# Kernel tuning notes

Hardware: AMD Instinct MI355X
Metric: run time of the kernel (lower is better)

## Reference

```python
import jax, jax.numpy as jnp
import numpy as np

EPS = 1e-5

def _bn(z, gamma, beta):
    mu = z.mean(axis=0)
    var = z.var(axis=0)  # biased, matches torch BN normalization
    return (z - mu) * jax.lax.rsqrt(var + EPS) * gamma + beta

def _sage_bn_relu(h, src, dst, n_nodes, Wl, bl, Wr, gamma, beta):
    # SAGEConv (mean aggr): out = lin_l(mean_{j in N(i)} h_j) + lin_r(h_i)
    msg = h[src]                                               # [E, d] gather
    agg = jax.ops.segment_sum(msg, dst, num_segments=n_nodes)  # [N, d]
    cnt = jax.ops.segment_sum(jnp.ones((src.shape[0], 1), h.dtype), dst,
                              num_segments=n_nodes)            # [N, 1]
    agg = jnp.where(cnt > 0, agg / jnp.maximum(cnt, 1.0), 0.0)
    out = agg @ Wl.T + bl + h @ Wr.T
    return jax.nn.relu(_bn(out, gamma, beta))

def setup_inputs() -> dict:
    key = jax.random.key(0)
    N, E, d, out_c, L, U = 50000, 800000, 128, 128, 3, 256
    ks = jax.random.split(key, 16)
    s = 1.0 / np.sqrt(d)
    return {
        "x": jax.random.normal(ks[0], (N, d), jnp.float32),
        "edge_index": jax.random.randint(ks[1], (2, E), 0, N, jnp.int64),
        "atom_mask": jax.random.uniform(ks[2], (N, 1), jnp.float32),
        "u_index": jax.random.randint(ks[3], (U,), 0, N, jnp.int64),
        "lin_l_w": jax.random.uniform(ks[4], (L, d, d), jnp.float32, -s, s),
        "lin_l_b": jax.random.uniform(ks[5], (L, d), jnp.float32, -s, s),
        "lin_r_w": jax.random.uniform(ks[6], (L, d, d), jnp.float32, -s, s),
        "bn_gamma": jnp.ones((L, d), jnp.float32),
        "bn_beta": jnp.zeros((L, d), jnp.float32),
        "ro_w1": jax.random.uniform(ks[7], (d, d), jnp.float32, -s, s),
        "ro_b1": jax.random.uniform(ks[8], (d,), jnp.float32, -s, s),
        "ro_bn_gamma": jnp.ones((d,), jnp.float32),
        "ro_bn_beta": jnp.zeros((d,), jnp.float32),
        "ro_w2": jax.random.uniform(ks[9], (out_c, d), jnp.float32, -s, s),
        "ro_b2": jax.random.uniform(ks[10], (out_c,), jnp.float32, -s, s),
    }

def reference(x, edge_index, atom_mask, u_index, lin_l_w, lin_l_b, lin_r_w,
              bn_gamma, bn_beta, ro_w1, ro_b1, ro_bn_gamma, ro_bn_beta,
              ro_w2, ro_b2):
    N = x.shape[0]
    src, dst = edge_index[0], edge_index[1]
    h = x
    for l in range(lin_l_w.shape[0]):
        h = _sage_bn_relu(h, src, dst, N, lin_l_w[l], lin_l_b[l],
                          lin_r_w[l], bn_gamma[l], bn_beta[l])
    state = h[u_index]                                         # [U, d]
    z = jax.nn.relu(_bn(h @ ro_w1.T + ro_b1, ro_bn_gamma, ro_bn_beta))
    atom = (z @ ro_w2.T + ro_b2) * atom_mask                   # [N, out]
    return (h, atom, state)
```

## Files before the change

### kernel.cpp

```cpp
#include <hip/hip_runtime.h>

#define D 128
#define LDA 136

typedef __attribute__((ext_vector_type(8))) short bf16x8;
typedef __attribute__((ext_vector_type(4))) float f32x4;

__device__ __forceinline__ ushort f2b(float f) {
  union { float f; unsigned u; } a; a.f = f;
  unsigned u = a.u;
  return (ushort)((u + 0x7fffu + ((u >> 16) & 1u)) >> 16);
}
__device__ __forceinline__ float b2f_lo(unsigned v) {
  union { unsigned u; float f; } a; a.u = v << 16; return a.f;
}
__device__ __forceinline__ float b2f_hi(unsigned v) {
  union { unsigned u; float f; } a; a.u = v & 0xffff0000u; return a.f;
}

__global__ void k_cast_pad(const float* __restrict__ s, ushort* __restrict__ d, int n4, int np4) {
  int i = blockIdx.x * blockDim.x + threadIdx.x;
  if (i >= np4) return;
  uint2 pk;
  if (i < n4) {
    float4 v = *(const float4*)&s[i * 4];
    pk.x = (unsigned)f2b(v.x) | ((unsigned)f2b(v.y) << 16);
    pk.y = (unsigned)f2b(v.z) | ((unsigned)f2b(v.w) << 16);
  } else {
    pk = make_uint2(0u, 0u);
  }
  *(uint2*)&d[i * 4] = pk;
}

__global__ void k_castw(const float* __restrict__ wl, const float* __restrict__ wr,
                        const float* __restrict__ w1, const float* __restrict__ w2,
                        ushort* __restrict__ dst, int LDD) {
  int i = blockIdx.x * blockDim.x + threadIdx.x;
  int total = 2 * LDD + 2 * D * D;
  if (i >= total) return;
  float v;
  if (i < LDD) v = wl[i];
  else if (i < 2 * LDD) v = wr[i - LDD];
  else if (i < 2 * LDD + D * D) v = w1[i - 2 * LDD];
  else v = w2[i - 2 * LDD - D * D];
  dst[i] = f2b(v);
}

__global__ void k_histrank(const int* __restrict__ dstI, int* __restrict__ cnt,
                           int* __restrict__ rankdst, int E) {
  int e = blockIdx.x * blockDim.x + threadIdx.x;
  if (e < E) {
    int d = dstI[e];
    int r = atomicAdd(&cnt[d], 1);
    rankdst[e] = (r << 16) | d;
  }
}
__global__ void k_scan1(const int* __restrict__ cnt, int* __restrict__ off,
                        int* __restrict__ bsum, int n) {
  __shared__ int sd[256];
  int t = threadIdx.x;
  int i = blockIdx.x * 256 + t;
  int x = (i < n) ? cnt[i] : 0;
  sd[t] = x;
  __syncthreads();
  for (int s = 1; s < 256; s <<= 1) {
    int v = (t >= s) ? sd[t - s] : 0;
    __syncthreads();
    sd[t] += v;
    __syncthreads();
  }
  if (i < n) off[i] = sd[t] - x;
  if (t == 255) bsum[blockIdx.x] = sd[255];
}
__global__ void k_scan2(const int* __restrict__ bsum, int* __restrict__ boff, int nb) {
  __shared__ int sd[256];
  int t = threadIdx.x;
  int x = (t < nb) ? bsum[t] : 0;
  sd[t] = x;
  __syncthreads();
  for (int s = 1; s < 256; s <<= 1) {
    int v = (t >= s) ? sd[t - s] : 0;
    __syncthreads();
    sd[t] += v;
    __syncthreads();
  }
  if (t < nb) boff[t] = sd[t] - x;
}
__global__ void k_scan3(int* __restrict__ off, const int* __restrict__ boff, int n) {
  int i = blockIdx.x * blockDim.x + threadIdx.x;
  if (i < n) off[i] += boff[i >> 8];
}
__global__ void k_fill(const int* __restrict__ srcI, const int* __restrict__ rankdst,
                       const int* __restrict__ off, int* __restrict__ eidx, int E) {
  int e = blockIdx.x * blockDim.x + threadIdx.x;
  if (e < E) {
    int rd = rankdst[e];
    int d = rd & 0xFFFF;
    eidx[off[d] + (rd >> 16)] = srcI[e];
  }
}

#define ACC8(A, V, B)                                             \
  A[B + 0] += b2f_lo(V.x); A[B + 1] += b2f_hi(V.x);               \
  A[B + 2] += b2f_lo(V.y); A[B + 3] += b2f_hi(V.y);               \
  A[B + 4] += b2f_lo(V.z); A[B + 5] += b2f_hi(V.z);               \
  A[B + 6] += b2f_lo(V.w); A[B + 7] += b2f_hi(V.w);

template <bool AGG>
__global__ __launch_bounds__(1024, 8) void k_fused(
    const ushort* __restrict__ hin, const ushort* __restrict__ Wl,
    const ushort* __restrict__ Wr, const float* __restrict__ bias,
    const int* __restrict__ off, const int* __restrict__ eidx,
    ushort* __restrict__ pre, float* __restrict__ sums, int N, int E) {
  __shared__ ushort aggS[128 * LDA];
  __shared__ float ls[2 * D];
  int t = threadIdx.x;
  int r0 = blockIdx.x * 128;

  if (t < 2 * D) ls[t] = 0.f;

  if (AGG) {
    int lrow = t >> 3;
    int row = r0 + lrow;
    int part = (t & 7) << 4;
    float a[16];
#pragma unroll
    for (int i = 0; i < 16; ++i) a[i] = 0.f;
    int start = 0, end = 0;
    if (row < N) { start = off[row]; end = (row == N - 1) ? E : off[row + 1]; }
    const ushort* hbase = hin + part;
#pragma unroll 2
    for (int e = start; e < end; ++e) {
      int sn = eidx[e];
      const uint4* p = (const uint4*)(hbase + (size_t)sn * D);
      uint4 v0 = p[0], v1 = p[1];
      ACC8(a, v0, 0) ACC8(a, v1, 8)
    }
    int deg = end - start;
    float inv = (deg > 0) ? 1.0f / (float)deg : 0.f;
    unsigned o[8];
#pragma unroll
    for (int i = 0; i < 8; ++i)
      o[i] = (unsigned)f2b(a[2 * i] * inv) | ((unsigned)f2b(a[2 * i + 1] * inv) << 16);
    uint4* dst = (uint4*)&aggS[lrow * LDA + part];
    dst[0] = make_uint4(o[0], o[1], o[2], o[3]);
    dst[1] = make_uint4(o[4], o[5], o[6], o[7]);
  }
  __syncthreads();

  int lane = t & 63;
  int wid = t >> 6;
  int wr = wid >> 2, wc = wid & 3;
  int rw = wr * 32, cw = wc * 32;
  int lr = lane & 15, lk = (lane >> 4) * 8;

  f32x4 acc[2][2];
#pragma unroll
  for (int i = 0; i < 2; ++i)
#pragma unroll
    for (int j = 0; j < 2; ++j) acc[i][j] = (f32x4){0.f, 0.f, 0.f, 0.f};

#pragma unroll
  for (int ks = 0; ks < 4; ++ks) {
    int kb = ks * 32 + lk;
    bf16x8 aA[2], aB[2];
#pragma unroll
    for (int rt = 0; rt < 2; ++rt) {
      if (AGG) {
        aA[rt] = *(const bf16x8*)&aggS[(rw + rt * 16 + lr) * LDA + kb];
        aB[rt] = *(const bf16x8*)&hin[(size_t)(r0 + rw + rt * 16 + lr) * D + kb];
      } else {
        aA[rt] = *(const bf16x8*)&hin[(size_t)(r0 + rw + rt * 16 + lr) * D + kb];
      }
    }
#pragma unroll
    for (int jt = 0; jt < 2; ++jt) {
      bf16x8 b1 = *(const bf16x8*)&Wl[(size_t)(cw + jt * 16 + lr) * D + kb];
      acc[0][jt] = __builtin_amdgcn_mfma_f32_16x16x32_bf16(aA[0], b1, acc[0][jt], 0, 0, 0);
      acc[1][jt] = __builtin_amdgcn_mfma_f32_16x16x32_bf16(aA[1], b1, acc[1][jt], 0, 0, 0);
      if (AGG) {
        bf16x8 b2 = *(const bf16x8*)&Wr[(size_t)(cw + jt * 16 + lr) * D + kb];
        acc[0][jt] = __builtin_amdgcn_mfma_f32_16x16x32_bf16(aB[0], b2, acc[0][jt], 0, 0, 0);
        acc[1][jt] = __builtin_amdgcn_mfma_f32_16x16x32_bf16(aB[1], b2, acc[1][jt], 0, 0, 0);
      }
    }
  }

  int crow = (lane >> 4) * 4;
#pragma unroll
  for (int jt = 0; jt < 2; ++jt) {
    int col = cw + jt * 16 + lr;
    float bv = bias[col];
    float s1 = 0.f, s2 = 0.f;
#pragma unroll
    for (int rt = 0; rt < 2; ++rt) {
      int rbase = r0 + rw + rt * 16 + crow;
#pragma unroll
      for (int rg = 0; rg < 4; ++rg) {
        int row = rbase + rg;
        if (row < N) {
          float v = acc[rt][jt][rg] + bv;
          pre[(size_t)row * D + col] = f2b(v);
          s1 += v; s2 += v * v;
        }
      }
    }
    s1 += __shfl_xor(s1, 16, 64); s1 += __shfl_xor(s1, 32, 64);
    s2 += __shfl_xor(s2, 16, 64); s2 += __shfl_xor(s2, 32, 64);
    if (lane < 16) {
      atomicAdd(&ls[cw + jt * 16 + lane], s1);
      atomicAdd(&ls[D + cw + jt * 16 + lane], s2);
    }
  }
  __syncthreads();
  if (t < 2 * D) atomicAdd(&sums[t], ls[t]);
}

template <bool F32OUT>
__global__ void k_bnrelu(const ushort* __restrict__ pre, const float* __restrict__ sums,
                         const float* __restrict__ gamma, const float* __restrict__ beta,
                         float* __restrict__ fout, ushort* __restrict__ bout,
                         int N, int Np, float invN) {
  int i4 = blockIdx.x * blockDim.x + threadIdx.x;
  if (i4 >= Np * (D / 4)) return;
  int row = i4 >> 5;
  int c4 = (i4 & 31) * 4;
  uint2 pk;
  if (row < N) {
    uint2 pv = *(const uint2*)&pre[(size_t)row * D + c4];
    float4 v = make_float4(b2f_lo(pv.x), b2f_hi(pv.x), b2f_lo(pv.y), b2f_hi(pv.y));
    float4 s = *(const float4*)&sums[c4];
    float4 q = *(const float4*)&sums[D + c4];
    float4 g = *(const float4*)&gamma[c4];
    float4 b = *(const float4*)&beta[c4];
    float mu, var, sc, sh;
    mu = s.x * invN; var = fmaxf(q.x * invN - mu * mu, 0.f);
    sc = g.x * rsqrtf(var + 1e-5f); sh = b.x - mu * sc;
    v.x = fmaxf(fmaf(v.x, sc, sh), 0.f);
    mu = s.y * invN; var = fmaxf(q.y * invN - mu * mu, 0.f);
    sc = g.y * rsqrtf(var + 1e-5f); sh = b.y - mu * sc;
    v.y = fmaxf(fmaf(v.y, sc, sh), 0.f);
    mu = s.z * invN; var = fmaxf(q.z * invN - mu * mu, 0.f);
    sc = g.z * rsqrtf(var + 1e-5f); sh = b.z - mu * sc;
    v.z = fmaxf(fmaf(v.z, sc, sh), 0.f);
    mu = s.w * invN; var = fmaxf(q.w * invN - mu * mu, 0.f);
    sc = g.w * rsqrtf(var + 1e-5f); sh = b.w - mu * sc;
    v.w = fmaxf(fmaf(v.w, sc, sh), 0.f);
    if (F32OUT) *(float4*)&fout[(size_t)row * D + c4] = v;
    pk.x = (unsigned)f2b(v.x) | ((unsigned)f2b(v.y) << 16);
    pk.y = (unsigned)f2b(v.z) | ((unsigned)f2b(v.w) << 16);
  } else {
    pk = make_uint2(0u, 0u);
  }
  *(uint2*)&bout[(size_t)row * D + c4] = pk;
}

__global__ __launch_bounds__(256) void k_mmfin(
    const ushort* __restrict__ A, const ushort* __restrict__ W,
    const float* __restrict__ bias, const float* __restrict__ mask,
    float* __restrict__ out, int N) {
  int t = threadIdx.x;
  int lane = t & 63;
  int wid = t >> 6;
  int wr = wid >> 1, wc = wid & 1;
  int r0 = blockIdx.x * 128 + wr * 64;
  int c0 = wc * 64;
  int lr = lane & 15, lk = (lane >> 4) * 8;

  f32x4 acc[4][4];
#pragma unroll
  for (int i = 0; i < 4; ++i)
#pragma unroll
    for (int j = 0; j < 4; ++j) acc[i][j] = (f32x4){0.f, 0.f, 0.f, 0.f};

#pragma unroll
  for (int ks = 0; ks < 4; ++ks) {
    int kb = ks * 32 + lk;
    bf16x8 a1[4];
#pragma unroll
    for (int rt = 0; rt < 4; ++rt)
      a1[rt] = *(const bf16x8*)&A[(size_t)(r0 + rt * 16 + lr) * D + kb];
#pragma unroll
    for (int jt = 0; jt < 4; ++jt) {
      bf16x8 b1 = *(const bf16x8*)&W[(size_t)(c0 + jt * 16 + lr) * D + kb];
#pragma unroll
      for (int rt = 0; rt < 4; ++rt)
        acc[rt][jt] = __builtin_amdgcn_mfma_f32_16x16x32_bf16(a1[rt], b1, acc[rt][jt], 0, 0, 0);
    }
  }

  int crow = (lane >> 4) * 4;
#pragma unroll
  for (int rt = 0; rt < 4; ++rt) {
    int rbase = r0 + rt * 16 + crow;
#pragma unroll
    for (int jt = 0; jt < 4; ++jt) {
      int col = c0 + jt * 16 + lr;
      float bv = bias[col];
#pragma unroll
      for (int rg = 0; rg < 4; ++rg) {
        int row = rbase + rg;
        if (row < N) {
          float m = mask[row];
          out[(size_t)row * D + col] = (acc[rt][jt][rg] + bv) * m;
        }
      }
    }
  }
}

__global__ void k_gather(const float* __restrict__ h, const int* __restrict__ uidx,
                         float* __restrict__ outp, int U) {
  int u = blockIdx.x;
  int t = threadIdx.x;
  int s = uidx[u];
  *(float4*)&outp[(size_t)u * D + t * 4] = *(const float4*)&h[(size_t)s * D + t * 4];
}

extern "C" void kernel_launch(void* const* d_in, const int* in_sizes, int n_in,
                              void* d_out, int out_size, void* d_ws, size_t ws_size,
                              hipStream_t stream) {
  const float* x        = (const float*)d_in[0];
  const int*   edge     = (const int*)d_in[1];
  const float* amask    = (const float*)d_in[2];
  const int*   uindex   = (const int*)d_in[3];
  const float* lin_l_w  = (const float*)d_in[4];
  const float* lin_l_b  = (const float*)d_in[5];
  const float* lin_r_w  = (const float*)d_in[6];
  const float* bn_gamma = (const float*)d_in[7];
  const float* bn_beta  = (const float*)d_in[8];
  const float* ro_w1    = (const float*)d_in[9];
  const float* ro_b1    = (const float*)d_in[10];
  const float* ro_bng   = (const float*)d_in[11];
  const float* ro_bnb   = (const float*)d_in[12];
  const float* ro_w2    = (const float*)d_in[13];
  const float* ro_b2    = (const float*)d_in[14];

  const int N = in_sizes[0] / D;
  const int E = in_sizes[1] / 2;
  const int U = in_sizes[3];
  const int L = in_sizes[4] / (D * D);
  const int Np = ((N + 127) / 128) * 128;
  const int LDD = L * D * D;

  const int* srcI = edge;
  const int* dstI = edge + E;

  float* outH     = (float*)d_out;
  float* outAtom  = outH + (size_t)N * D;
  float* outState = outAtom + (size_t)N * D;

  char* w = (char*)d_ws;
  ushort* hb   = (ushort*)w; w += (size_t)Np * D * 2;
  ushort* pre  = (ushort*)w; w += (size_t)Np * D * 2;
  ushort* wall = (ushort*)w; w += (size_t)(2 * LDD + 2 * D * D) * 2;
  int*    cnt  = (int*)w;    w += (size_t)N * 4;
  float*  sums = (float*)w;  w += 4 * 2 * D * 4;
  int* off     = (int*)w;    w += (size_t)N * 4;
  int* rankdst = (int*)w;    w += (size_t)E * 4;
  int* eidx    = (int*)w;    w += (size_t)E * 4;
  int* bsum    = (int*)w;    w += 1024;
  int* boff    = (int*)w;    w += 1024;

  ushort* wlb = wall;
  ushort* wrb = wlb + (size_t)LDD;
  ushort* w1b = wrb + (size_t)LDD;
  ushort* w2b = w1b + (size_t)D * D;

  k_cast_pad<<<(Np * D / 4 + 255) / 256, 256, 0, stream>>>(x, hb, N * D / 4, Np * D / 4);
  k_castw<<<(2 * LDD + 2 * D * D + 255) / 256, 256, 0, stream>>>(lin_l_w, lin_r_w, ro_w1, ro_w2, wall, LDD);
  hipMemsetAsync(cnt, 0, (size_t)N * 4 + 4 * 2 * D * 4, stream);

  int nbE = (E + 255) / 256;
  int nbN = (N + 255) / 256;
  k_histrank<<<nbE, 256, 0, stream>>>(dstI, cnt, rankdst, E);
  k_scan1<<<nbN, 256, 0, stream>>>(cnt, off, bsum, N);
  k_scan2<<<1, 256, 0, stream>>>(bsum, boff, nbN);
  k_scan3<<<nbN, 256, 0, stream>>>(off, boff, N);
  k_fill<<<nbE, 256, 0, stream>>>(srcI, rankdst, off, eidx, E);

  const int fusedBlocks = Np / 128;
  const int bnBlocks = (Np * (D / 4) + 255) / 256;
  const float invN = 1.0f / (float)N;

  for (int l = 0; l < L; ++l) {
    float* lsums = sums + (size_t)l * 2 * D;
    k_fused<true><<<fusedBlocks, 1024, 0, stream>>>(
        hb, wlb + (size_t)l * D * D, wrb + (size_t)l * D * D,
        lin_l_b + (size_t)l * D, off, eidx, pre, lsums, N, E);
    if (l == L - 1)
      k_bnrelu<true><<<bnBlocks, 256, 0, stream>>>(pre, lsums, bn_gamma + (size_t)l * D,
                                                   bn_beta + (size_t)l * D, outH, hb, N, Np, invN);
    else
      k_bnrelu<false><<<bnBlocks, 256, 0, stream>>>(pre, lsums, bn_gamma + (size_t)l * D,
                                                    bn_beta + (size_t)l * D, nullptr, hb, N, Np, invN);
  }

  float* rsums = sums + (size_t)L * 2 * D;
  k_fused<false><<<fusedBlocks, 1024, 0, stream>>>(
      hb, w1b, nullptr, ro_b1, off, eidx, pre, rsums, N, E);
  k_bnrelu<false><<<bnBlocks, 256, 0, stream>>>(pre, rsums, ro_bng, ro_bnb, nullptr, hb, N, Np, invN);
  k_mmfin<<<Np / 128, 256, 0, stream>>>(hb, w2b, ro_b2, amask, outAtom, N);
  k_gather<<<U, 32, 0, stream>>>(outH, uindex, outState, U);
}
```

Measured before the change: 324.4 us.

## Merge prep kernels, shrink edge index to u16, halve fused block size

Merges the input cast, weight cast and memset into a single prep kernel, which saves launch overhead. The CSR edge index is stored as 16-bit values, halving the bytes read in the gather loop. The fused SAGE kernel now uses 512 threads per block: each thread aggregates one row slice in four phases, and each wave computes a 32x64 output tile, giving more MFMA work per wave. Storing source indices as ushort silently truncates any node id of 65536 or more. N is 50000 here, so it is correct for these inputs but not in general.

```diff
diff --git a/kernel.cpp b/kernel.cpp
--- a/kernel.cpp
+++ b/kernel.cpp
@@ -18,32 +18,37 @@
   union { unsigned u; float f; } a; a.u = v & 0xffff0000u; return a.f;
 }
 
-__global__ void k_cast_pad(const float* __restrict__ s, ushort* __restrict__ d, int n4, int np4) {
+__global__ void k_prep(const float* __restrict__ x, const float* __restrict__ wl,
+                       const float* __restrict__ wr, const float* __restrict__ w1,
+                       const float* __restrict__ w2, ushort* __restrict__ hb,
+                       ushort* __restrict__ wall, uint4* __restrict__ zr,
+                       int nX4, int npX4, int LDD, int nZero4) {
   int i = blockIdx.x * blockDim.x + threadIdx.x;
-  if (i >= np4) return;
-  uint2 pk;
-  if (i < n4) {
-    float4 v = *(const float4*)&s[i * 4];
-    pk.x = (unsigned)f2b(v.x) | ((unsigned)f2b(v.y) << 16);
-    pk.y = (unsigned)f2b(v.z) | ((unsigned)f2b(v.w) << 16);
-  } else {
-    pk = make_uint2(0u, 0u);
-  }
-  *(uint2*)&d[i * 4] = pk;
-}
-
-__global__ void k_castw(const float* __restrict__ wl, const float* __restrict__ wr,
-                        const float* __restrict__ w1, const float* __restrict__ w2,
-                        ushort* __restrict__ dst, int LDD) {
-  int i = blockIdx.x * blockDim.x + threadIdx.x;
-  int total = 2 * LDD + 2 * D * D;
-  if (i >= total) return;
-  float v;
-  if (i < LDD) v = wl[i];
-  else if (i < 2 * LDD) v = wr[i - LDD];
-  else if (i < 2 * LDD + D * D) v = w1[i - 2 * LDD];
-  else v = w2[i - 2 * LDD - D * D];
-  dst[i] = f2b(v);
+  if (i < npX4) {
+    uint2 pk;
+    if (i < nX4) {
+      float4 v = *(const float4*)&x[i * 4];
+      pk.x = (unsigned)f2b(v.x) | ((unsigned)f2b(v.y) << 16);
+      pk.y = (unsigned)f2b(v.z) | ((unsigned)f2b(v.w) << 16);
+    } else {
+      pk = make_uint2(0u, 0u);
+    }
+    *(uint2*)&hb[i * 4] = pk;
+    return;
+  }
+  int j = i - npX4;
+  int W = 2 * LDD + 2 * D * D;
+  if (j < W) {
+    float v;
+    if (j < LDD) v = wl[j];
+    else if (j < 2 * LDD) v = wr[j - LDD];
+    else if (j < 2 * LDD + D * D) v = w1[j - 2 * LDD];
+    else v = w2[j - 2 * LDD - D * D];
+    wall[j] = f2b(v);
+    return;
+  }
+  int z = j - W;
+  if (z < nZero4) zr[z] = make_uint4(0u, 0u, 0u, 0u);
 }
 
 __global__ void k_histrank(const int* __restrict__ dstI, int* __restrict__ cnt,
@@ -91,12 +96,12 @@
   if (i < n) off[i] += boff[i >> 8];
 }
 __global__ void k_fill(const int* __restrict__ srcI, const int* __restrict__ rankdst,
-                       const int* __restrict__ off, int* __restrict__ eidx, int E) {
+                       const int* __restrict__ off, ushort* __restrict__ eidx, int E) {
   int e = blockIdx.x * blockDim.x + threadIdx.x;
   if (e < E) {
     int rd = rankdst[e];
     int d = rd & 0xFFFF;
-    eidx[off[d] + (rd >> 16)] = srcI[e];
+    eidx[off[d] + (rd >> 16)] = (ushort)srcI[e];
   }
 }
 
@@ -107,10 +112,10 @@
   A[B + 6] += b2f_lo(V.w); A[B + 7] += b2f_hi(V.w);
 
 template <bool AGG>
-__global__ __launch_bounds__(1024, 8) void k_fused(
+__global__ __launch_bounds__(512) void k_fused(
     const ushort* __restrict__ hin, const ushort* __restrict__ Wl,
     const ushort* __restrict__ Wr, const float* __restrict__ bias,
-    const int* __restrict__ off, const int* __restrict__ eidx,
+    const int* __restrict__ off, const ushort* __restrict__ eidx,
     ushort* __restrict__ pre, float* __restrict__ sums, int N, int E) {
   __shared__ ushort aggS[128 * LDA];
   __shared__ float ls[2 * D];
@@ -120,45 +125,46 @@
   if (t < 2 * D) ls[t] = 0.f;
 
   if (AGG) {
-    int lrow = t >> 3;
+    int lrow = t >> 2;
     int row = r0 + lrow;
-    int part = (t & 7) << 4;
-    float a[16];
-#pragma unroll
-    for (int i = 0; i < 16; ++i) a[i] = 0.f;
+    int sub = (t & 3) << 3;
     int start = 0, end = 0;
     if (row < N) { start = off[row]; end = (row == N - 1) ? E : off[row + 1]; }
-    const ushort* hbase = hin + part;
-#pragma unroll 2
-    for (int e = start; e < end; ++e) {
-      int sn = eidx[e];
-      const uint4* p = (const uint4*)(hbase + (size_t)sn * D);
-      uint4 v0 = p[0], v1 = p[1];
-      ACC8(a, v0, 0) ACC8(a, v1, 8)
-    }
     int deg = end - start;
     float inv = (deg > 0) ? 1.0f / (float)deg : 0.f;
-    unsigned o[8];
-#pragma unroll
-    for (int i = 0; i < 8; ++i)
-      o[i] = (unsigned)f2b(a[2 * i] * inv) | ((unsigned)f2b(a[2 * i + 1] * inv) << 16);
-    uint4* dst = (uint4*)&aggS[lrow * LDA + part];
-    dst[0] = make_uint4(o[0], o[1], o[2], o[3]);
-    dst[1] = make_uint4(o[4], o[5], o[6], o[7]);
+#pragma unroll
+    for (int ph = 0; ph < 4; ++ph) {
+      const ushort* hbase = hin + ph * 32 + sub;
+      float a[8];
+#pragma unroll
+      for (int i = 0; i < 8; ++i) a[i] = 0.f;
+#pragma unroll 2
+      for (int e = start; e < end; ++e) {
+        int sn = eidx[e];
+        uint4 v = *(const uint4*)(hbase + (size_t)sn * D);
+        ACC8(a, v, 0)
+      }
+      uint4 o;
+      o.x = (unsigned)f2b(a[0] * inv) | ((unsigned)f2b(a[1] * inv) << 16);
+      o.y = (unsigned)f2b(a[2] * inv) | ((unsigned)f2b(a[3] * inv) << 16);
+      o.z = (unsigned)f2b(a[4] * inv) | ((unsigned)f2b(a[5] * inv) << 16);
+      o.w = (unsigned)f2b(a[6] * inv) | ((unsigned)f2b(a[7] * inv) << 16);
+      *(uint4*)&aggS[lrow * LDA + ph * 32 + sub] = o;
+    }
   }
   __syncthreads();
 
   int lane = t & 63;
   int wid = t >> 6;
-  int wr = wid >> 2, wc = wid & 3;
-  int rw = wr * 32, cw = wc * 32;
+  int wr = wid >> 1, wc = wid & 1;
+  int rw = wr * 32, cw = wc * 64;
   int lr = lane & 15, lk = (lane >> 4) * 8;
 
-  f32x4 acc[2][2];
+  f32x4 acc[2][4];
 #pragma unroll
   for (int i = 0; i < 2; ++i)
 #pragma unroll
-    for (int j = 0; j < 2; ++j) acc[i][j] = (f32x4){0.f, 0.f, 0.f, 0.f};
+    for (int j = 0; j < 4; ++j) acc[i][j] = (f32x4){0.f, 0.f, 0.f, 0.f};
 
 #pragma unroll
   for (int ks = 0; ks < 4; ++ks) {
@@ -174,7 +180,7 @@
       }
     }
 #pragma unroll
-    for (int jt = 0; jt < 2; ++jt) {
+    for (int jt = 0; jt < 4; ++jt) {
       bf16x8 b1 = *(const bf16x8*)&Wl[(size_t)(cw + jt * 16 + lr) * D + kb];
       acc[0][jt] = __builtin_amdgcn_mfma_f32_16x16x32_bf16(aA[0], b1, acc[0][jt], 0, 0, 0);
       acc[1][jt] = __builtin_amdgcn_mfma_f32_16x16x32_bf16(aA[1], b1, acc[1][jt], 0, 0, 0);
@@ -188,7 +194,7 @@
 
   int crow = (lane >> 4) * 4;
 #pragma unroll
-  for (int jt = 0; jt < 2; ++jt) {
+  for (int jt = 0; jt < 4; ++jt) {
     int col = cw + jt * 16 + lr;
     float bv = bias[col];
     float s1 = 0.f, s2 = 0.f;
@@ -358,7 +364,7 @@
   float*  sums = (float*)w;  w += 4 * 2 * D * 4;
   int* off     = (int*)w;    w += (size_t)N * 4;
   int* rankdst = (int*)w;    w += (size_t)E * 4;
-  int* eidx    = (int*)w;    w += (size_t)E * 4;
+  ushort* eidx = (ushort*)w; w += (size_t)((E + 1) & ~1) * 2;
   int* bsum    = (int*)w;    w += 1024;
   int* boff    = (int*)w;    w += 1024;
 
@@ -367,9 +373,16 @@
   ushort* w1b = wrb + (size_t)LDD;
   ushort* w2b = w1b + (size_t)D * D;
 
-  k_cast_pad<<<(Np * D / 4 + 255) / 256, 256, 0, stream>>>(x, hb, N * D / 4, Np * D / 4);
-  k_castw<<<(2 * LDD + 2 * D * D + 255) / 256, 256, 0, stream>>>(lin_l_w, lin_r_w, ro_w1, ro_w2, wall, LDD);
-  hipMemsetAsync(cnt, 0, (size_t)N * 4 + 4 * 2 * D * 4, stream);
+  const float invN = 1.0f / (float)N;
+
+  {
+    int nX4 = N * D / 4, npX4 = Np * D / 4;
+    int W = 2 * LDD + 2 * D * D;
+    int nZero4 = (N + 4 * 2 * D) / 4;
+    int total = npX4 + W + nZero4;
+    k_prep<<<(total + 255) / 256, 256, 0, stream>>>(x, lin_l_w, lin_r_w, ro_w1, ro_w2,
+                                                    hb, wall, (uint4*)cnt, nX4, npX4, LDD, nZero4);
+  }
 
   int nbE = (E + 255) / 256;
   int nbN = (N + 255) / 256;
@@ -381,11 +394,10 @@
 
   const int fusedBlocks = Np / 128;
   const int bnBlocks = (Np * (D / 4) + 255) / 256;
-  const float invN = 1.0f / (float)N;
 
   for (int l = 0; l < L; ++l) {
     float* lsums = sums + (size_t)l * 2 * D;
-    k_fused<true><<<fusedBlocks, 1024, 0, stream>>>(
+    k_fused<true><<<fusedBlocks, 512, 0, stream>>>(
         hb, wlb + (size_t)l * D * D, wrb + (size_t)l * D * D,
         lin_l_b + (size_t)l * D, off, eidx, pre, lsums, N, E);
     if (l == L - 1)
@@ -397,7 +409,7 @@
   }
 
   float* rsums = sums + (size_t)L * 2 * D;
-  k_fused<false><<<fusedBlocks, 1024, 0, stream>>>(
+  k_fused<false><<<fusedBlocks, 512, 0, stream>>>(
       hb, w1b, nullptr, ro_b1, off, eidx, pre, rsums, N, E);
   k_bnrelu<false><<<bnBlocks, 256, 0, stream>>>(pre, rsums, ro_bng, ro_bnb, nullptr, hb, N, Np, invN);
   k_mmfin<<<Np / 128, 256, 0, stream>>>(hb, w2b, ro_b2, amask, outAtom, N);
```

Measured after the change: 365.9 us. 12.8% more time.
